# Kernel optimization log

Hardware: AMD Instinct MI355X
Metric: run time of the kernel (lower is better)

## Reference

```python
import jax, jax.numpy as jnp
import numpy as np

T, H = 4096, 2048


def setup_inputs() -> dict:
    key = jax.random.key(0)
    k_a, k_b, k_x = jax.random.split(key, 3)
    # glorot-style init matching the module: uniform(-1,1) * sqrt(2/sum(shape))
    a = jax.random.uniform(k_a, (H,), minval=-1.0, maxval=1.0) * jnp.sqrt(2.0 / H)
    B = jax.random.uniform(k_b, (H, H), minval=-1.0, maxval=1.0) * jnp.sqrt(2.0 / (2 * H))
    x = jax.random.normal(k_x, (T, H), dtype=jnp.float32)
    return {"x": x, "a": a, "B": B}


def reference(x, a, B):
    # x: (T, H); per-timestep s_t = B.T @ x_t  ->  s = x @ B, laid out NCH = (1, H, T)
    Tl, Hl = x.shape
    s = jnp.einsum("th,hk->kt", x, B)[None]  # (1, H, T)
    # depthwise causal kernel: k[h, t] = a[h]**t, time as final dim, flipped for conv
    exponents = jnp.arange(Tl)
    kernel = jnp.power(a[:, None], exponents)          # (H, T)
    kernel_flipped = jnp.flip(kernel, axis=-1)[:, None, :]  # (H, 1, T) OIH
    s_padded = jnp.pad(s, ((0, 0), (0, 0), (Tl - 1, 0)))    # causal left-pad
    conv_out = jax.lax.conv_general_dilated(
        s_padded, kernel_flipped,
        window_strides=(1,), padding="VALID",
        dimension_numbers=("NCH", "OIH", "NCH"),
        feature_group_count=Hl,
    )  # (1, H, T): h_t[h] = sum_{k<=t} a[h]**(t-k) * s_k[h]
    return jnp.transpose(conv_out, (0, 2, 1))  # (1, T, H)
```

## Files before the change

### kernel.cpp

```cpp
#include <hip/hip_runtime.h>
#include <stdint.h>

#define TDIM 4096
#define HDIM 2048

#define BM 128
#define BN 128
#define BK 32

typedef short short8 __attribute__((ext_vector_type(8)));
typedef float f32x4 __attribute__((ext_vector_type(4)));

__device__ __forceinline__ uint16_t f2bf(float f) {
  uint32_t u = __builtin_bit_cast(uint32_t, f);
  u += 0x7fffu + ((u >> 16) & 1u);
  return (uint16_t)(u >> 16);
}
__device__ __forceinline__ float bf2f(uint32_t h) {
  uint32_t u = h << 16;
  return __builtin_bit_cast(float, u);
}

__device__ __forceinline__ void async_copy16(const void* gsrc, void* ldst) {
  __builtin_amdgcn_global_load_lds(
      (const __attribute__((address_space(1))) uint32_t*)gsrc,
      (__attribute__((address_space(3))) uint32_t*)ldst,
      16, 0, 0);
}

__global__ void cvt_x(const float* __restrict__ in, uint16_t* __restrict__ out) {
  size_t i = ((size_t)blockIdx.x * 256 + threadIdx.x) * 8;
  float4 v0 = *(const float4*)(in + i);
  float4 v1 = *(const float4*)(in + i + 4);
  union { uint16_t h[8]; uint4 v; } o;
  o.h[0] = f2bf(v0.x); o.h[1] = f2bf(v0.y); o.h[2] = f2bf(v0.z); o.h[3] = f2bf(v0.w);
  o.h[4] = f2bf(v1.x); o.h[5] = f2bf(v1.y); o.h[6] = f2bf(v1.z); o.h[7] = f2bf(v1.w);
  *(uint4*)(out + i) = o.v;
}

__global__ void transpose_cvt(const float* __restrict__ B, uint16_t* __restrict__ Bt) {
  __shared__ uint16_t tile[64][65];
  const int k0 = blockIdx.y * 64;
  const int n0 = blockIdx.x * 64;
  const int tid = threadIdx.x;
  for (int i = 0; i < 16; ++i) {
    int idx = i * 256 + tid;
    int r = idx >> 6, c = idx & 63;
    tile[r][c] = f2bf(B[(size_t)(k0 + r) * HDIM + n0 + c]);
  }
  __syncthreads();
  for (int i = 0; i < 16; ++i) {
    int idx = i * 256 + tid;
    int r = idx >> 6, c = idx & 63;
    Bt[(size_t)(n0 + r) * HDIM + k0 + c] = tile[c][r];
  }
}

__global__ __launch_bounds__(512) void gemm_bf16(
    const uint16_t* __restrict__ A, const uint16_t* __restrict__ Bt,
    uint16_t* __restrict__ S) {
  __shared__ __align__(16) uint16_t As[BM * BK];
  __shared__ __align__(16) uint16_t Bs[BN * BK];

  const int tid  = threadIdx.x;
  const int lane = tid & 63;
  const int wave = tid >> 6;
  const int wm = (wave >> 2) * 64;
  const int wn = (wave & 3) * 32;
  const int m0 = blockIdx.y * BM;
  const int n0 = blockIdx.x * BN;

  f32x4 acc[4][2] = {};

  const int rloc  = lane >> 2;
  const int swzl  = (rloc & 3) ^ ((rloc >> 2) & 3);
  const int gchunk = (lane & 3) ^ swzl;
  const char* aptr = (const char*)A +
      ((size_t)(m0 + wave * 16 + rloc) * HDIM + gchunk * 8) * 2;
  const char* bptr = (const char*)Bt +
      ((size_t)(n0 + wave * 16 + rloc) * HDIM + gchunk * 8) * 2;
  char* As_base = (char*)As + wave * 1024;
  char* Bs_base = (char*)Bs + wave * 1024;

  const int fr = lane & 15;
  const int fq = lane >> 4;
  const int swzf = (fr & 3) ^ ((fr >> 2) & 3);
  const int rchunk = fq ^ swzf;

  for (int kt = 0; kt < HDIM / BK; ++kt) {
    __syncthreads();
    async_copy16(aptr, As_base);
    async_copy16(bptr, Bs_base);
    aptr += BK * 2;
    bptr += BK * 2;
    asm volatile("s_waitcnt vmcnt(0)" ::: "memory");
    __syncthreads();

    short8 af[4], bfr[2];
#pragma unroll
    for (int im = 0; im < 4; ++im)
      af[im] = *(const short8*)&As[(wm + im * 16 + fr) * BK + rchunk * 8];
#pragma unroll
    for (int in = 0; in < 2; ++in)
      bfr[in] = *(const short8*)&Bs[(wn + in * 16 + fr) * BK + rchunk * 8];
#pragma unroll
    for (int im = 0; im < 4; ++im)
#pragma unroll
      for (int in = 0; in < 2; ++in)
        acc[im][in] = __builtin_amdgcn_mfma_f32_16x16x32_bf16(
            af[im], bfr[in], acc[im][in], 0, 0, 0);
  }

#pragma unroll
  for (int im = 0; im < 4; ++im) {
#pragma unroll
    for (int in = 0; in < 2; ++in) {
      int col  = n0 + wn + in * 16 + fr;
      int rowb = m0 + wm + im * 16 + fq * 4;
#pragma unroll
      for (int r = 0; r < 4; ++r)
        S[(size_t)(rowb + r) * HDIM + col] = f2bf(acc[im][in][r]);
    }
  }
}

#define TT 16
#define WARM 16
__global__ void conv_scan(const uint16_t* __restrict__ S, const float* __restrict__ a,
                          float* __restrict__ out) {
  const int h  = (blockIdx.x * 256 + threadIdx.x) * 4;
  const int t0 = blockIdx.y * TT;
  const float4 av = *(const float4*)(a + h);
  float a0 = 0.f, a1 = 0.f, a2 = 0.f, a3 = 0.f;
  if (t0 > 0) {
#pragma unroll
    for (int i = 0; i < WARM; ++i) {
      int t = t0 - WARM + i;
      uint2 sv = *(const uint2*)(S + (size_t)t * HDIM + h);
      a0 = av.x * a0 + bf2f(sv.x & 0xffffu);
      a1 = av.y * a1 + bf2f(sv.x >> 16);
      a2 = av.z * a2 + bf2f(sv.y & 0xffffu);
      a3 = av.w * a3 + bf2f(sv.y >> 16);
    }
  }
#pragma unroll
  for (int i = 0; i < TT; ++i) {
    int t = t0 + i;
    uint2 sv = *(const uint2*)(S + (size_t)t * HDIM + h);
    a0 = av.x * a0 + bf2f(sv.x & 0xffffu);
    a1 = av.y * a1 + bf2f(sv.x >> 16);
    a2 = av.z * a2 + bf2f(sv.y & 0xffffu);
    a3 = av.w * a3 + bf2f(sv.y >> 16);
    float4 o = make_float4(a0, a1, a2, a3);
    *(float4*)(out + (size_t)t * HDIM + h) = o;
  }
}

extern "C" void kernel_launch(void* const* d_in, const int* in_sizes, int n_in,
                              void* d_out, int out_size, void* d_ws, size_t ws_size,
                              hipStream_t stream) {
  const float* x = (const float*)d_in[0];
  const float* a = (const float*)d_in[1];
  const float* B = (const float*)d_in[2];
  float* out = (float*)d_out;

  uint16_t* xb  = (uint16_t*)d_ws;
  uint16_t* Btb = (uint16_t*)((char*)d_ws + (size_t)16 * 1024 * 1024);
  uint16_t* S   = (uint16_t*)((char*)d_ws + (size_t)24 * 1024 * 1024);

  cvt_x<<<(TDIM * HDIM) / (8 * 256), 256, 0, stream>>>(x, xb);
  transpose_cvt<<<dim3(HDIM / 64, HDIM / 64), 256, 0, stream>>>(B, Btb);
  gemm_bf16<<<dim3(HDIM / BN, TDIM / BM), 512, 0, stream>>>(xb, Btb, S);
  conv_scan<<<dim3(HDIM / (256 * 4), TDIM / TT), 256, 0, stream>>>(S, a, out);
}
```

Baseline: 152.2 us.

## Double-buffer GEMM LDS tiles with BK=64 and fuse input prep kernels

The GEMM now uses BK=64 with two LDS buffers and issues the next tile's async global-to-LDS loads before computing the current one. Synchronisation is a partial vmcnt wait plus raw barriers, with an 8-way XOR swizzle for the wider rows. The x conversion and the B transpose/convert are merged into one launch, and the transpose now uses vectorised loads and stores. This aims to hide global load latency, halve the number of barriers, and remove one launch, at the cost of more LDS per block, which may limit occupancy.

```diff
diff --git a/kernel.cpp b/kernel.cpp
--- a/kernel.cpp
+++ b/kernel.cpp
@@ -6,7 +6,7 @@
 
 #define BM 128
 #define BN 128
-#define BK 32
+#define BK 64
 
 typedef short short8 __attribute__((ext_vector_type(8)));
 typedef float f32x4 __attribute__((ext_vector_type(4)));
@@ -28,39 +28,55 @@
       16, 0, 0);
 }
 
-__global__ void cvt_x(const float* __restrict__ in, uint16_t* __restrict__ out) {
-  size_t i = ((size_t)blockIdx.x * 256 + threadIdx.x) * 8;
-  float4 v0 = *(const float4*)(in + i);
-  float4 v1 = *(const float4*)(in + i + 4);
-  union { uint16_t h[8]; uint4 v; } o;
-  o.h[0] = f2bf(v0.x); o.h[1] = f2bf(v0.y); o.h[2] = f2bf(v0.z); o.h[3] = f2bf(v0.w);
-  o.h[4] = f2bf(v1.x); o.h[5] = f2bf(v1.y); o.h[6] = f2bf(v1.z); o.h[7] = f2bf(v1.w);
-  *(uint4*)(out + i) = o.v;
-}
-
-__global__ void transpose_cvt(const float* __restrict__ B, uint16_t* __restrict__ Bt) {
-  __shared__ uint16_t tile[64][65];
-  const int k0 = blockIdx.y * 64;
-  const int n0 = blockIdx.x * 64;
-  const int tid = threadIdx.x;
-  for (int i = 0; i < 16; ++i) {
-    int idx = i * 256 + tid;
-    int r = idx >> 6, c = idx & 63;
-    tile[r][c] = f2bf(B[(size_t)(k0 + r) * HDIM + n0 + c]);
-  }
-  __syncthreads();
-  for (int i = 0; i < 16; ++i) {
-    int idx = i * 256 + tid;
-    int r = idx >> 6, c = idx & 63;
-    Bt[(size_t)(n0 + r) * HDIM + k0 + c] = tile[c][r];
-  }
-}
-
-__global__ __launch_bounds__(512) void gemm_bf16(
+__global__ void prep(const float* __restrict__ x, const float* __restrict__ B,
+                     uint16_t* __restrict__ xb, uint16_t* __restrict__ Bt) {
+  __shared__ uint16_t tile[64][68];
+  const int t = threadIdx.x;
+  if (blockIdx.x < 4096) {
+    size_t i = ((size_t)blockIdx.x * 256 + t) * 8;
+    float4 v0 = *(const float4*)(x + i);
+    float4 v1 = *(const float4*)(x + i + 4);
+    union { uint16_t h[8]; uint4 v; } o;
+    o.h[0] = f2bf(v0.x); o.h[1] = f2bf(v0.y); o.h[2] = f2bf(v0.z); o.h[3] = f2bf(v0.w);
+    o.h[4] = f2bf(v1.x); o.h[5] = f2bf(v1.y); o.h[6] = f2bf(v1.z); o.h[7] = f2bf(v1.w);
+    *(uint4*)(xb + i) = o.v;
+  } else {
+    const int bid = blockIdx.x - 4096;
+    const int n0 = (bid & 31) * 64;
+    const int k0 = (bid >> 5) * 64;
+    {
+      const int r  = t >> 4;
+      const int c4 = (t & 15) * 4;
+#pragma unroll
+      for (int i = 0; i < 4; ++i) {
+        int rr = r + i * 16;
+        float4 v = *(const float4*)&B[(size_t)(k0 + rr) * HDIM + n0 + c4];
+        union { uint16_t h[4]; uint2 u; } o;
+        o.h[0] = f2bf(v.x); o.h[1] = f2bf(v.y); o.h[2] = f2bf(v.z); o.h[3] = f2bf(v.w);
+        *(uint2*)&tile[rr][c4] = o.u;
+      }
+    }
+    __syncthreads();
+    {
+      const int nr = t >> 2;
+      const int kc = (t & 3) * 4;
+#pragma unroll
+      for (int i = 0; i < 4; ++i) {
+        int kk = kc + i * 16;
+        union { uint16_t h[4]; uint2 u; } o;
+        o.h[0] = tile[kk][nr];     o.h[1] = tile[kk + 1][nr];
+        o.h[2] = tile[kk + 2][nr]; o.h[3] = tile[kk + 3][nr];
+        *(uint2*)&Bt[(size_t)(n0 + nr) * HDIM + k0 + kk] = o.u;
+      }
+    }
+  }
+}
+
+__global__ __launch_bounds__(512, 4) void gemm_bf16(
     const uint16_t* __restrict__ A, const uint16_t* __restrict__ Bt,
     uint16_t* __restrict__ S) {
-  __shared__ __align__(16) uint16_t As[BM * BK];
-  __shared__ __align__(16) uint16_t Bs[BN * BK];
+  __shared__ __align__(16) uint16_t As[2][BM * BK];
+  __shared__ __align__(16) uint16_t Bs[2][BN * BK];
 
   const int tid  = threadIdx.x;
   const int lane = tid & 63;
@@ -72,44 +88,59 @@
 
   f32x4 acc[4][2] = {};
 
-  const int rloc  = lane >> 2;
-  const int swzl  = (rloc & 3) ^ ((rloc >> 2) & 3);
-  const int gchunk = (lane & 3) ^ swzl;
-  const char* aptr = (const char*)A +
-      ((size_t)(m0 + wave * 16 + rloc) * HDIM + gchunk * 8) * 2;
-  const char* bptr = (const char*)Bt +
-      ((size_t)(n0 + wave * 16 + rloc) * HDIM + gchunk * 8) * 2;
-  char* As_base = (char*)As + wave * 1024;
-  char* Bs_base = (char*)Bs + wave * 1024;
+  const int lr = lane >> 3;
+  const int gc = (lane & 7) ^ lr;
+  const char* aA0 = (const char*)A  + ((size_t)(m0 + wave * 16 + lr)     * HDIM + gc * 8) * 2;
+  const char* aA1 = (const char*)A  + ((size_t)(m0 + wave * 16 + 8 + lr) * HDIM + gc * 8) * 2;
+  const char* aB0 = (const char*)Bt + ((size_t)(n0 + wave * 16 + lr)     * HDIM + gc * 8) * 2;
+  const char* aB1 = (const char*)Bt + ((size_t)(n0 + wave * 16 + 8 + lr) * HDIM + gc * 8) * 2;
 
   const int fr = lane & 15;
   const int fq = lane >> 4;
-  const int swzf = (fr & 3) ^ ((fr >> 2) & 3);
-  const int rchunk = fq ^ swzf;
-
-  for (int kt = 0; kt < HDIM / BK; ++kt) {
-    __syncthreads();
-    async_copy16(aptr, As_base);
-    async_copy16(bptr, Bs_base);
-    aptr += BK * 2;
-    bptr += BK * 2;
-    asm volatile("s_waitcnt vmcnt(0)" ::: "memory");
-    __syncthreads();
-
-    short8 af[4], bfr[2];
-#pragma unroll
-    for (int im = 0; im < 4; ++im)
-      af[im] = *(const short8*)&As[(wm + im * 16 + fr) * BK + rchunk * 8];
-#pragma unroll
-    for (int in = 0; in < 2; ++in)
-      bfr[in] = *(const short8*)&Bs[(wn + in * 16 + fr) * BK + rchunk * 8];
-#pragma unroll
-    for (int im = 0; im < 4; ++im)
-#pragma unroll
-      for (int in = 0; in < 2; ++in)
-        acc[im][in] = __builtin_amdgcn_mfma_f32_16x16x32_bf16(
-            af[im], bfr[in], acc[im][in], 0, 0, 0);
-  }
+
+#define ISSUE(kt, b)                                                        \
+  do {                                                                      \
+    size_t koff = (size_t)(kt) * (BK * 2);                                  \
+    char* dA = (char*)As + (b) * 16384 + (wave * 16) * 128;                 \
+    char* dB = (char*)Bs + (b) * 16384 + (wave * 16) * 128;                 \
+    async_copy16(aA0 + koff, dA);                                           \
+    async_copy16(aA1 + koff, dA + 1024);                                    \
+    async_copy16(aB0 + koff, dB);                                           \
+    async_copy16(aB1 + koff, dB + 1024);                                    \
+  } while (0)
+
+  ISSUE(0, 0);
+  const int NKT = HDIM / BK;
+  for (int kt = 0; kt < NKT; ++kt) {
+    int nkt = (kt + 1 < NKT) ? kt + 1 : kt;
+    ISSUE(nkt, (kt + 1) & 1);
+    asm volatile("s_waitcnt vmcnt(4)\n\ts_barrier" ::: "memory");
+
+    const uint16_t* as = &As[kt & 1][0];
+    const uint16_t* bs = &Bs[kt & 1][0];
+#pragma unroll
+    for (int s = 0; s < 2; ++s) {
+      short8 af[4], bfr[2];
+#pragma unroll
+      for (int im = 0; im < 4; ++im) {
+        int row = wm + im * 16 + fr;
+        af[im] = *(const short8*)&as[row * 64 + (((s * 4 + fq) ^ (row & 7)) * 8)];
+      }
+#pragma unroll
+      for (int in = 0; in < 2; ++in) {
+        int row = wn + in * 16 + fr;
+        bfr[in] = *(const short8*)&bs[row * 64 + (((s * 4 + fq) ^ (row & 7)) * 8)];
+      }
+#pragma unroll
+      for (int im = 0; im < 4; ++im)
+#pragma unroll
+        for (int in = 0; in < 2; ++in)
+          acc[im][in] = __builtin_amdgcn_mfma_f32_16x16x32_bf16(
+              af[im], bfr[in], acc[im][in], 0, 0, 0);
+    }
+    asm volatile("s_barrier" ::: "memory");
+  }
+#undef ISSUE
 
 #pragma unroll
   for (int im = 0; im < 4; ++im) {
@@ -168,8 +199,7 @@
   uint16_t* Btb = (uint16_t*)((char*)d_ws + (size_t)16 * 1024 * 1024);
   uint16_t* S   = (uint16_t*)((char*)d_ws + (size_t)24 * 1024 * 1024);
 
-  cvt_x<<<(TDIM * HDIM) / (8 * 256), 256, 0, stream>>>(x, xb);
-  transpose_cvt<<<dim3(HDIM / 64, HDIM / 64), 256, 0, stream>>>(B, Btb);
+  prep<<<4096 + 1024, 256, 0, stream>>>(x, B, xb, Btb);
   gemm_bf16<<<dim3(HDIM / BN, TDIM / BM), 512, 0, stream>>>(xb, Btb, S);
   conv_scan<<<dim3(HDIM / (256 * 4), TDIM / TT), 256, 0, stream>>>(S, a, out);
 }
```

Result: faster. 140.4 us (-7.8%).
